# Performance work log

Hardware: AMD Instinct MI355X
Metric: run time of the kernel (lower is better)

Reference implementation:

```python
import jax, jax.numpy as jnp
import numpy as np

VOCAB, D, H1, H2, T = 32000, 256, 256, 256, 12
PAD, START, STOP = 0, 10, 11
B, S, NS = 32, 512, 16


def setup_inputs() -> dict:
    key = jax.random.key(0)
    ks = jax.random.split(key, 16)
    def rn(k, shape, scale=0.1):
        return (jax.random.normal(k, shape) * scale).astype(jnp.float32)
    inputs = jax.random.randint(ks[0], (B, S), 0, VOCAB)
    sent_embs = jax.random.normal(ks[1], (B, NS, 2 * H1), dtype=jnp.float32)
    embed = rn(ks[2], (VOCAB, D)).at[0].set(0.0)  # padding_idx=0
    # BiLSTM 1: input D, hidden H1; gate order i,f,g,o; dim 0 = [fwd, bwd]
    lstm1_wih = rn(ks[3], (2, 4 * H1, D))
    lstm1_whh = rn(ks[4], (2, 4 * H1, H1))
    lstm1_b = rn(ks[5], (2, 4 * H1))  # b_ih + b_hh fused
    # BiLSTM 2: input 4*H1 (= 2*2*lstm1_units), hidden H2
    lstm2_wih = rn(ks[6], (2, 4 * H2, 4 * H1))
    lstm2_whh = rn(ks[7], (2, 4 * H2, H2))
    lstm2_b = rn(ks[8], (2, 4 * H2))
    attW = rn(ks[9], (2 * H1, 2 * H1))
    h2t_w = rn(ks[10], (T, 2 * H2))
    h2t_b = rn(ks[11], (T,))
    trans = jax.random.normal(ks[12], (T, T), dtype=jnp.float32)
    trans = trans.at[START, :].set(-10000.0).at[:, STOP].set(-10000.0)
    return dict(inputs=inputs, sent_embs=sent_embs, embed=embed,
                lstm1_wih=lstm1_wih, lstm1_whh=lstm1_whh, lstm1_b=lstm1_b,
                lstm2_wih=lstm2_wih, lstm2_whh=lstm2_whh, lstm2_b=lstm2_b,
                attW=attW, h2t_w=h2t_w, h2t_b=h2t_b, trans=trans)


def _lstm_dir(x, wih, whh, b, reverse=False):
    # x: (S, B, Din) -> (S, B, H)
    if reverse:
        x = x[::-1]
    Hh = whh.shape[1]
    Bn = x.shape[1]
    def step(carry, xt):
        h, c = carry
        gates = xt @ wih.T + h @ whh.T + b
        i, f, g, o = jnp.split(gates, 4, axis=-1)
        c = jax.nn.sigmoid(f) * c + jax.nn.sigmoid(i) * jnp.tanh(g)
        h = jax.nn.sigmoid(o) * jnp.tanh(c)
        return (h, c), h
    init = (jnp.zeros((Bn, Hh), x.dtype), jnp.zeros((Bn, Hh), x.dtype))
    _, hs = jax.lax.scan(step, init, x)
    return hs[::-1] if reverse else hs


def _bilstm(x, wih, whh, b):
    fwd = _lstm_dir(x, wih[0], whh[0], b[0])
    bwd = _lstm_dir(x, wih[1], whh[1], b[1], reverse=True)
    return jnp.concatenate([fwd, bwd], axis=-1)


def _lstm_features(inputs, sent_embs, embed, lstm1_wih, lstm1_whh, lstm1_b,
                   lstm2_wih, lstm2_whh, lstm2_b, attW, h2t_w, h2t_b):
    emb = embed[inputs].transpose(1, 0, 2)            # (S,B,D); dropout is identity at eval
    l1 = _bilstm(emb, lstm1_wih, lstm1_whh, lstm1_b)  # (S,B,2H1)
    word = l1.transpose(1, 0, 2)                      # (B,S,2H1)
    wx = jnp.einsum('bse,fe->bsf', word, attW)        # Linear W (no bias)
    scores = jnp.einsum('bsf,bnf->bsn', wx, sent_embs)
    aw = jax.nn.softmax(scores, axis=-1)
    g = jnp.einsum('bsn,bnf->bsf', aw, sent_embs)
    comb = jnp.concatenate([wx, g], axis=-1)          # (B,S,4H1)
    l2 = _bilstm(comb.transpose(1, 0, 2), lstm2_wih, lstm2_whh, lstm2_b)  # (S,B,2H2)
    feats = jnp.einsum('sbf,tf->bst', l2, h2t_w) + h2t_b  # (B,S,T)
    return feats


def _viterbi(feats_b, trans):
    # feats_b: (S,T) -> (path (S,), score)
    init = jnp.full((T,), -10000.0, feats_b.dtype).at[START].set(0.0)
    def step(fv, feat):
        sc = fv[None, :] + trans          # [next, prev]
        bp = jnp.argmax(sc, axis=1)
        return jnp.max(sc, axis=1) + feat, bp
    fv, bps = jax.lax.scan(step, init, feats_b)
    term = fv + trans[STOP]
    best = jnp.argmax(term)
    def back(tag, bp):
        return bp[tag], tag
    _, path = jax.lax.scan(back, best, bps, reverse=True)
    return path, term[best]


def reference(inputs, sent_embs, embed, lstm1_wih, lstm1_whh, lstm1_b,
              lstm2_wih, lstm2_whh, lstm2_b, attW, h2t_w, h2t_b, trans):
    feats = _lstm_features(inputs, sent_embs, embed, lstm1_wih, lstm1_whh, lstm1_b,
                           lstm2_wih, lstm2_whh, lstm2_b, attW, h2t_w, h2t_b)
    paths, _ = jax.vmap(_viterbi, in_axes=(0, None))(feats, trans)
    return paths  # (B,S) predicted tag sequence
```

## Files before the change

kernel.cpp:

```cpp
#include <hip/hip_runtime.h>
#include <hip/hip_bf16.h>

#define BB 32
#define SS 512
#define DD 256
#define HH 256
#define GG 1024
#define MM (SS*BB)
#define NSENT 16
#define TT 12
#define TAG_START 10
#define TAG_STOP 11

typedef unsigned long long u64;
typedef unsigned int u32;

__device__ __forceinline__ float sigm(float x) {
  x = fminf(fmaxf(x, -15.f), 15.f);
  return 1.f / (1.f + __expf(-x));
}
__device__ __forceinline__ float tanh_fast(float x) {
  x = fminf(fmaxf(x, -15.f), 15.f);
  float e = __expf(2.f * x);
  return (e - 1.f) / (e + 1.f);
}

__global__ void embed_kernel(const int* __restrict__ toks, const float* __restrict__ emb,
                             float* __restrict__ X1) {
  int m = blockIdx.x;
  int s = m >> 5, b = m & 31;
  int tok = toks[b * SS + s];
  ((float4*)(X1 + (size_t)m * DD))[threadIdx.x] =
      ((const float4*)(emb + (size_t)tok * DD))[threadIdx.x];
}

__launch_bounds__(256)
__global__ void gemm_nt(const float* __restrict__ A, const float* __restrict__ W_,
                        const float* __restrict__ bias_, float* __restrict__ C_,
                        int K, int lda, int ldw, int ldC, size_t wz, size_t cz) {
  __shared__ float As[16 * 132];
  __shared__ float Ws[16 * 132];
  const float* W = W_ + (size_t)blockIdx.z * wz;
  const float* bias = bias_ ? bias_ + (size_t)blockIdx.z * GG : nullptr;
  float* C = C_ + (size_t)blockIdx.z * cz;
  const int tid = threadIdx.x;
  const int n0 = blockIdx.x * 128, m0 = blockIdx.y * 128;
  const int row = tid & 127, half = tid >> 7;
  const int tx = tid & 15, ty = tid >> 4;
  float acc[8][8] = {};
  const float* Arow = A + (size_t)(m0 + row) * lda;
  const float* Wrow = W + (size_t)(n0 + row) * ldw;
  for (int kk = 0; kk < K; kk += 16) {
    const int kb = half * 8;
    float4 a0 = *(const float4*)(Arow + kk + kb);
    float4 a1 = *(const float4*)(Arow + kk + kb + 4);
    float4 w0 = *(const float4*)(Wrow + kk + kb);
    float4 w1 = *(const float4*)(Wrow + kk + kb + 4);
    As[(kb + 0) * 132 + row] = a0.x; As[(kb + 1) * 132 + row] = a0.y;
    As[(kb + 2) * 132 + row] = a0.z; As[(kb + 3) * 132 + row] = a0.w;
    As[(kb + 4) * 132 + row] = a1.x; As[(kb + 5) * 132 + row] = a1.y;
    As[(kb + 6) * 132 + row] = a1.z; As[(kb + 7) * 132 + row] = a1.w;
    Ws[(kb + 0) * 132 + row] = w0.x; Ws[(kb + 1) * 132 + row] = w0.y;
    Ws[(kb + 2) * 132 + row] = w0.z; Ws[(kb + 3) * 132 + row] = w0.w;
    Ws[(kb + 4) * 132 + row] = w1.x; Ws[(kb + 5) * 132 + row] = w1.y;
    Ws[(kb + 6) * 132 + row] = w1.z; Ws[(kb + 7) * 132 + row] = w1.w;
    __syncthreads();
#pragma unroll
    for (int kl = 0; kl < 16; ++kl) {
      const float4 alo = *(const float4*)&As[kl * 132 + ty * 4];
      const float4 ahi = *(const float4*)&As[kl * 132 + 64 + ty * 4];
      const float4 wlo = *(const float4*)&Ws[kl * 132 + tx * 4];
      const float4 whi = *(const float4*)&Ws[kl * 132 + 64 + tx * 4];
      const float am[8] = {alo.x, alo.y, alo.z, alo.w, ahi.x, ahi.y, ahi.z, ahi.w};
      const float wm[8] = {wlo.x, wlo.y, wlo.z, wlo.w, whi.x, whi.y, whi.z, whi.w};
#pragma unroll
      for (int i = 0; i < 8; ++i)
#pragma unroll
        for (int j = 0; j < 8; ++j) acc[i][j] = fmaf(am[i], wm[j], acc[i][j]);
    }
    __syncthreads();
  }
  float4 blo = make_float4(0.f, 0.f, 0.f, 0.f), bhi = blo;
  if (bias) {
    blo = *(const float4*)(bias + n0 + tx * 4);
    bhi = *(const float4*)(bias + n0 + 64 + tx * 4);
  }
#pragma unroll
  for (int i = 0; i < 8; ++i) {
    const int m = m0 + ((i < 4) ? (ty * 4 + i) : (64 + ty * 4 + i - 4));
    float4 lo = make_float4(acc[i][0] + blo.x, acc[i][1] + blo.y,
                            acc[i][2] + blo.z, acc[i][3] + blo.w);
    float4 hi = make_float4(acc[i][4] + bhi.x, acc[i][5] + bhi.y,
                            acc[i][6] + bhi.z, acc[i][7] + bhi.w);
    *(float4*)(C + (size_t)m * ldC + n0 + tx * 4) = lo;
    *(float4*)(C + (size_t)m * ldC + n0 + 64 + tx * 4) = hi;
  }
}

__global__ void prep_whh(const float* __restrict__ whh1, const float* __restrict__ whh2,
                         float* __restrict__ o1, float* __restrict__ o2) {
  int idx0 = blockIdx.x * 256 + threadIdx.x;
  int layer = idx0 >> 19;
  int idx = idx0 & 524287;
  const float* whh = layer ? whh2 : whh1;
  float* out = layer ? o2 : o1;
  int c    = idx & 3;
  int t    = (idx >> 2) & 255;
  int i4   = (idx >> 10) & 31;
  int sl   = (idx >> 15) & 7;
  int d    = idx >> 18;
  int r    = t & 127;
  int half = t >> 7;
  int g = (r >> 5) * 256 + sl * 32 + (r & 31);
  int k = half * 128 + i4 * 4 + c;
  out[idx] = whh[(size_t)(d * GG + g) * HH + k];
}

__launch_bounds__(256, 1)
__global__ void rec_kernel(const float* __restrict__ Xp, const float* __restrict__ whh_p,
                           float* __restrict__ hist, u64* __restrict__ hx,
                           const float* __restrict__ aw, const float* __restrict__ sentW,
                           int useAtt) {
  __shared__ float h_lds[512];
  __shared__ float p_lds[512];
  const int tid = threadIdx.x;
  const int bid = blockIdx.x;
  const int sl = bid >> 5;
  const int db = bid & 31;
  const int d = db & 1;
  const int bg = db >> 1;
  const int r = tid & 127;
  const int half = tid >> 7;
  const float* wp = whh_p + (size_t)(d * 8 + sl) * 32768;
  float w[128];
#pragma unroll
  for (int i4 = 0; i4 < 32; ++i4) {
    const float4 v = *(const float4*)&wp[(size_t)(i4 * 256 + tid) * 4];
    w[i4 * 4 + 0] = v.x; w[i4 * 4 + 1] = v.y;
    w[i4 * 4 + 2] = v.z; w[i4 * 4 + 3] = v.w;
  }
  const float* XpD = Xp + (size_t)d * MM * GG;
  const int gcol = (r >> 5) * 256 + sl * 32 + (r & 31);
  const int jj = tid & 31, cc = tid >> 5;
  const int histMine = ((r >> 4) == sl);
  float creg = 0.f;
  float swA[8], swB[8];
  if (useAtt) {
    const float* swp = sentW + ((size_t)d * 512 + (size_t)(bg * 2) * 16) * 1024 + gcol;
#pragma unroll
    for (int n = 0; n < 8; ++n) {
      swA[n] = swp[(size_t)(half * 8 + n) * 1024];
      swB[n] = swp[(size_t)(16 + half * 8 + n) * 1024];
    }
  }
  u64* grp[2] = { hx + ((size_t)(0 * 2 + d) * 16 + bg) * 512,
                  hx + ((size_t)(1 * 2 + d) * 16 + bg) * 512 };
#pragma unroll 1
  for (int t = 0; t < SS; ++t) {
    const int s = d ? (SS - 1 - t) : t;
    const int m0 = s * BB + bg * 2;
    float x0 = 0.f, x1 = 0.f;
    if (half == 0) {
      x0 = XpD[(size_t)m0 * GG + gcol];
      x1 = XpD[(size_t)(m0 + 1) * GG + gcol];
    }
    if (useAtt) {
      const float* a0 = aw + (size_t)m0 * 16 + half * 8;
#pragma unroll
      for (int n = 0; n < 8; ++n) {
        x0 = fmaf(a0[n], swA[n], x0);
        x1 = fmaf(a0[16 + n], swB[n], x1);
      }
    }
    u64 w0, w1;
    {
      u64* base = grp[t & 1] + tid * 2;
      w0 = __hip_atomic_load(base + 0, __ATOMIC_RELAXED, __HIP_MEMORY_SCOPE_AGENT);
      w1 = __hip_atomic_load(base + 1, __ATOMIC_RELAXED, __HIP_MEMORY_SCOPE_AGENT);
      while (((u32)(w0 >> 32) != (u32)t) | ((u32)(w1 >> 32) != (u32)t)) {
        __builtin_amdgcn_s_sleep(1);
        w0 = __hip_atomic_load(base + 0, __ATOMIC_RELAXED, __HIP_MEMORY_SCOPE_AGENT);
        w1 = __hip_atomic_load(base + 1, __ATOMIC_RELAXED, __HIP_MEMORY_SCOPE_AGENT);
      }
    }
    *(float2*)&h_lds[tid * 2] = make_float2(__uint_as_float((u32)w0),
                                            __uint_as_float((u32)w1));
    if (histMine && t > 0) {
      const int sp = d ? (SS - t) : (t - 1);
      *(float2*)&hist[(size_t)(sp * BB + bg * 2 + half) * 512 + d * 256 + r * 2] =
          make_float2(__uint_as_float((u32)w0), __uint_as_float((u32)w1));
    }
    __syncthreads();
    {
      const int kb = half * 128;
      float p0a = 0.f, p0b = 0.f, p1a = 0.f, p1b = 0.f;
#pragma unroll
      for (int k8 = 0; k8 < 16; ++k8) {
        const float4 h0a = *(const float4*)&h_lds[kb + k8 * 8];
        const float4 h0b = *(const float4*)&h_lds[kb + k8 * 8 + 4];
        const float4 h1a = *(const float4*)&h_lds[256 + kb + k8 * 8];
        const float4 h1b = *(const float4*)&h_lds[256 + kb + k8 * 8 + 4];
        p0a = fmaf(w[k8*8+0], h0a.x, p0a); p0a = fmaf(w[k8*8+1], h0a.y, p0a);
        p0a = fmaf(w[k8*8+2], h0a.z, p0a); p0a = fmaf(w[k8*8+3], h0a.w, p0a);
        p0b = fmaf(w[k8*8+4], h0b.x, p0b); p0b = fmaf(w[k8*8+5], h0b.y, p0b);
        p0b = fmaf(w[k8*8+6], h0b.z, p0b); p0b = fmaf(w[k8*8+7], h0b.w, p0b);
        p1a = fmaf(w[k8*8+0], h1a.x, p1a); p1a = fmaf(w[k8*8+1], h1a.y, p1a);
        p1a = fmaf(w[k8*8+2], h1a.z, p1a); p1a = fmaf(w[k8*8+3], h1a.w, p1a);
        p1b = fmaf(w[k8*8+4], h1b.x, p1b); p1b = fmaf(w[k8*8+5], h1b.y, p1b);
        p1b = fmaf(w[k8*8+6], h1b.z, p1b); p1b = fmaf(w[k8*8+7], h1b.w, p1b);
      }
      *(float2*)&p_lds[tid * 2] = make_float2(p0a + p0b + x0, p1a + p1b + x1);
    }
    __syncthreads();
    if (tid < 64) {
      const float iv = p_lds[(jj) * 2 + cc]       + p_lds[(128 + jj) * 2 + cc];
      const float fv = p_lds[(32 + jj) * 2 + cc]  + p_lds[(128 + 32 + jj) * 2 + cc];
      const float gv = p_lds[(64 + jj) * 2 + cc]  + p_lds[(128 + 64 + jj) * 2 + cc];
      const float ov = p_lds[(96 + jj) * 2 + cc]  + p_lds[(128 + 96 + jj) * 2 + cc];
      const float cs = sigm(fv) * creg + sigm(iv) * tanh_fast(gv);
      creg = cs;
      const float hn = sigm(ov) * tanh_fast(cs);
      u64 wv = ((u64)(u32)(t + 1) << 32) | (u64)__float_as_uint(hn);
      __hip_atomic_store(grp[(t + 1) & 1] + cc * 256 + sl * 32 + jj, wv,
                         __ATOMIC_RELAXED, __HIP_MEMORY_SCOPE_AGENT);
    }
  }
  if (histMine) {
    u64* base = grp[SS & 1] + tid * 2;
    u64 w0, w1;
    do {
      w0 = __hip_atomic_load(base + 0, __ATOMIC_RELAXED, __HIP_MEMORY_SCOPE_AGENT);
      w1 = __hip_atomic_load(base + 1, __ATOMIC_RELAXED, __HIP_MEMORY_SCOPE_AGENT);
      if (((u32)(w0 >> 32) == (u32)SS) & ((u32)(w1 >> 32) == (u32)SS)) break;
      __builtin_amdgcn_s_sleep(1);
    } while (true);
    const int sp = d ? 0 : (SS - 1);
    *(float2*)&hist[(size_t)(sp * BB + bg * 2 + half) * 512 + d * 256 + r * 2] =
        make_float2(__uint_as_float((u32)w0), __uint_as_float((u32)w1));
  }
}

__global__ void aw_kernel(const float* __restrict__ wx, const float* __restrict__ sent,
                          float* __restrict__ awout) {
  __shared__ float sl[NSENT * 512];
  __shared__ float wxr[512];
  __shared__ float parts[256];
  __shared__ float avals[NSENT];
  __shared__ float red0;
  const int tid = threadIdx.x;
  const int b = blockIdx.y;
  const int s0 = blockIdx.x * 32;
  for (int i = tid; i < NSENT * 512; i += 256) sl[i] = sent[(size_t)b * NSENT * 512 + i];
  __syncthreads();
  for (int si = 0; si < 32; ++si) {
    const int m = (s0 + si) * BB + b;
    for (int i = tid; i < 512; i += 256) wxr[i] = wx[(size_t)m * 512 + i];
    __syncthreads();
    const int n = tid >> 4, kp = tid & 15;
    float p = 0.f;
#pragma unroll 8
    for (int f = kp * 32; f < kp * 32 + 32; ++f) p = fmaf(wxr[f], sl[n * 512 + f], p);
    parts[tid] = p;
    __syncthreads();
    if (tid < NSENT) {
      float sc = 0.f;
      for (int qq = 0; qq < 16; ++qq) sc += parts[tid * 16 + qq];
      avals[tid] = sc;
    }
    __syncthreads();
    if (tid == 0) {
      float mx = avals[0];
      for (int qq = 1; qq < NSENT; ++qq) mx = fmaxf(mx, avals[qq]);
      float sm = 0.f;
      for (int qq = 0; qq < NSENT; ++qq) { float e = expf(avals[qq] - mx); avals[qq] = e; sm += e; }
      red0 = 1.f / sm;
    }
    __syncthreads();
    if (tid < NSENT) awout[(size_t)m * 16 + tid] = avals[tid] * red0;
    __syncthreads();
  }
}

__global__ void feats_kernel(const float* __restrict__ l2m, const float* __restrict__ w,
                             const float* __restrict__ bias, float* __restrict__ feats) {
  const int wave = threadIdx.x >> 6, lane = threadIdx.x & 63;
  const int m = blockIdx.x * 4 + wave;
  const float* row = l2m + (size_t)m * 512;
  float rv[8];
#pragma unroll
  for (int i = 0; i < 8; ++i) rv[i] = row[lane + i * 64];
  for (int t = 0; t < TT; ++t) {
    const float* wr = w + t * 512;
    float p = 0.f;
#pragma unroll
    for (int i = 0; i < 8; ++i) p = fmaf(rv[i], wr[lane + i * 64], p);
#pragma unroll
    for (int off = 32; off; off >>= 1) p += __shfl_down(p, off);
    if (lane == 0) feats[(size_t)m * TT + t] = p + bias[t];
  }
}

__global__ void viterbi_kernel(const float* __restrict__ feats, const float* __restrict__ trans,
                               int* __restrict__ out) {
  __shared__ float flds[SS * TT];
  __shared__ unsigned char bp[SS * TT];
  __shared__ float tr[TT * TT];
  __shared__ float fv[TT];
  __shared__ float tv[TT];
  __shared__ int pathS[SS];
  const int b = blockIdx.x, tid = threadIdx.x;
  for (int i = tid; i < SS * TT; i += 64) {
    int s = i / TT, t = i - s * TT;
    flds[i] = feats[(size_t)(s * BB + b) * TT + t];
  }
  for (int i = tid; i < TT * TT; i += 64) tr[i] = trans[i];
  if (tid < TT) fv[tid] = (tid == TAG_START) ? 0.f : -10000.f;
  __syncthreads();
  for (int s = 0; s < SS; ++s) {
    float nf = 0.f;
    if (tid < TT) {
      float mx = -1e30f;
      int bj = 0;
#pragma unroll
      for (int jj = 0; jj < TT; ++jj) {
        float v = fv[jj] + tr[tid * TT + jj];
        if (v > mx) { mx = v; bj = jj; }
      }
      nf = mx + flds[s * TT + tid];
      bp[s * TT + tid] = (unsigned char)bj;
    }
    __syncthreads();
    if (tid < TT) fv[tid] = nf;
    __syncthreads();
  }
  if (tid < TT) tv[tid] = fv[tid] + tr[TAG_STOP * TT + tid];
  __syncthreads();
  if (tid == 0) {
    int best = 0;
    float mx = tv[0];
    for (int jj = 1; jj < TT; ++jj)
      if (tv[jj] > mx) { mx = tv[jj]; best = jj; }
    pathS[SS - 1] = best;
    for (int s = SS - 1; s > 0; --s) { best = bp[s * TT + best]; pathS[s - 1] = best; }
  }
  __syncthreads();
  for (int s = tid; s < SS; s += 64) out[b * SS + s] = pathS[s];
}

#define OFF_XP    ((size_t)0)
#define OFF_WX    ((size_t)134217728)
#define OFF_L2M   ((size_t)167772160)
#define OFF_WORD  ((size_t)201326592)
#define OFF_WT1   ((size_t)234881024)
#define OFF_WT2   ((size_t)236978176)
#define OFF_FEATS ((size_t)239075328)
#define OFF_HX1   ((size_t)239861760)
#define OFF_HX2   ((size_t)240123904)
#define OFF_SENTW ((size_t)240386048)
#define OFF_AW    ((size_t)244580352)

extern "C" void kernel_launch(void* const* d_in, const int* in_sizes, int n_in,
                              void* d_out, int out_size, void* d_ws, size_t ws_size,
                              hipStream_t stream) {
  const int* inputs  = (const int*)d_in[0];
  const float* sent  = (const float*)d_in[1];
  const float* emb   = (const float*)d_in[2];
  const float* l1wih = (const float*)d_in[3];
  const float* l1whh = (const float*)d_in[4];
  const float* l1b   = (const float*)d_in[5];
  const float* l2wih = (const float*)d_in[6];
  const float* l2whh = (const float*)d_in[7];
  const float* l2b   = (const float*)d_in[8];
  const float* attW  = (const float*)d_in[9];
  const float* h2tw  = (const float*)d_in[10];
  const float* h2tb  = (const float*)d_in[11];
  const float* trans = (const float*)d_in[12];
  int* out = (int*)d_out;
  char* ws = (char*)d_ws;

  float* Xp    = (float*)(ws + OFF_XP);
  float* wx    = (float*)(ws + OFF_WX);
  float* l2m   = (float*)(ws + OFF_L2M);
  float* X1    = l2m;
  float* word  = (float*)(ws + OFF_WORD);
  float* wt1   = (float*)(ws + OFF_WT1);
  float* wt2   = (float*)(ws + OFF_WT2);
  float* feats = (float*)(ws + OFF_FEATS);
  u64* hx1     = (u64*)(ws + OFF_HX1);
  u64* hx2     = (u64*)(ws + OFF_HX2);
  float* sentW = (float*)(ws + OFF_SENTW);
  float* awb   = (float*)(ws + OFF_AW);

  (void)hipMemsetAsync(ws + OFF_HX1, 0, 262144 * 2, stream);

  prep_whh<<<4096, 256, 0, stream>>>(l1whh, l2whh, wt1, wt2);
  gemm_nt<<<dim3(8, 4, 2), 256, 0, stream>>>(sent, l2wih + 512, nullptr, sentW,
                                             512, 512, GG, 1024,
                                             (size_t)GG * GG, (size_t)512 * 1024);
  embed_kernel<<<MM, 64, 0, stream>>>(inputs, emb, X1);
  gemm_nt<<<dim3(8, 128, 2), 256, 0, stream>>>(X1, l1wih, l1b, Xp,
                                               DD, DD, DD, GG,
                                               (size_t)GG * DD, (size_t)MM * GG);
  rec_kernel<<<256, 256, 0, stream>>>(Xp, wt1, word, hx1, nullptr, nullptr, 0);
  gemm_nt<<<dim3(4, 128, 1), 256, 0, stream>>>(word, attW, nullptr, wx,
                                               512, 512, 512, 512, 0, 0);
  aw_kernel<<<dim3(16, 32), 256, 0, stream>>>(wx, sent, awb);
  gemm_nt<<<dim3(8, 128, 2), 256, 0, stream>>>(wx, l2wih, l2b, Xp,
                                               512, 512, GG, GG,
                                               (size_t)GG * GG, (size_t)MM * GG);
  rec_kernel<<<256, 256, 0, stream>>>(Xp, wt2, l2m, hx2, awb, sentW, 1);
  feats_kernel<<<MM / 4, 256, 0, stream>>>(l2m, h2tw, h2tb, feats);
  viterbi_kernel<<<BB, 64, 0, stream>>>(feats, trans, out);
}
```

Baseline: 3.931 ms.

## Process four batch rows per recurrent block and hoist attention add out of recurrence

The recurrent LSTM kernel now handles four batch rows per block instead of two, cutting the grid from 256 to 128 blocks so each step's weight-register reuse doubles and fewer blocks take part in the cross-block handshake. The attention-weighted sentence term is moved out of the serial loop into a separate parallel kernel that adds it into Xp beforehand. The loop also prefetches the next step's Xp inputs, has one wave poll the hidden-state exchange with wide vectorized loads, and uses raw barriers. The cost is an extra pass over Xp and double the FMA work per block on the critical path.

```diff
diff --git a/kernel.cpp b/kernel.cpp
--- a/kernel.cpp
+++ b/kernel.cpp
@@ -116,19 +116,42 @@
   out[idx] = whh[(size_t)(d * GG + g) * HH + k];
 }
 
+__global__ void attadd_kernel(const float* __restrict__ aw, const float* __restrict__ sentW,
+                              float* __restrict__ Xp) {
+  __shared__ float a[NSENT];
+  const int idx = blockIdx.x;
+  const int d = idx >> 14;
+  const int m = idx & (MM - 1);
+  const int b = m & 31;
+  const int tid = threadIdx.x;
+  if (tid < NSENT) a[tid] = aw[(size_t)m * 16 + tid];
+  __syncthreads();
+  const int g = tid * 4;
+  float* xp = Xp + ((size_t)d * MM + m) * GG + g;
+  const float* swp = sentW + ((size_t)d * 512 + b * 16) * 1024 + g;
+  float4 acc = *(const float4*)xp;
+#pragma unroll
+  for (int n = 0; n < NSENT; ++n) {
+    const float4 sw = *(const float4*)&swp[(size_t)n * 1024];
+    acc.x = fmaf(a[n], sw.x, acc.x);
+    acc.y = fmaf(a[n], sw.y, acc.y);
+    acc.z = fmaf(a[n], sw.z, acc.z);
+    acc.w = fmaf(a[n], sw.w, acc.w);
+  }
+  *(float4*)xp = acc;
+}
+
 __launch_bounds__(256, 1)
 __global__ void rec_kernel(const float* __restrict__ Xp, const float* __restrict__ whh_p,
-                           float* __restrict__ hist, u64* __restrict__ hx,
-                           const float* __restrict__ aw, const float* __restrict__ sentW,
-                           int useAtt) {
-  __shared__ float h_lds[512];
-  __shared__ float p_lds[512];
+                           float* __restrict__ hist, u64* __restrict__ hx) {
+  __shared__ float h_lds[1024];
+  __shared__ float p_lds[1024];
   const int tid = threadIdx.x;
   const int bid = blockIdx.x;
-  const int sl = bid >> 5;
-  const int db = bid & 31;
+  const int sl = bid >> 4;
+  const int db = bid & 15;
   const int d = db & 1;
-  const int bg = db >> 1;
+  const int bq = db >> 1;
   const int r = tid & 127;
   const int half = tid >> 7;
   const float* wp = whh_p + (size_t)(d * 8 + sl) * 32768;
@@ -141,102 +164,148 @@
   }
   const float* XpD = Xp + (size_t)d * MM * GG;
   const int gcol = (r >> 5) * 256 + sl * 32 + (r & 31);
-  const int jj = tid & 31, cc = tid >> 5;
-  const int histMine = ((r >> 4) == sl);
+  const int etid = tid - 128;
+  const int ecc = (etid >= 0) ? (etid >> 5) : 0;
+  const int ejj = etid & 31;
   float creg = 0.f;
-  float swA[8], swB[8];
-  if (useAtt) {
-    const float* swp = sentW + ((size_t)d * 512 + (size_t)(bg * 2) * 16) * 1024 + gcol;
-#pragma unroll
-    for (int n = 0; n < 8; ++n) {
-      swA[n] = swp[(size_t)(half * 8 + n) * 1024];
-      swB[n] = swp[(size_t)(16 + half * 8 + n) * 1024];
-    }
-  }
-  u64* grp[2] = { hx + ((size_t)(0 * 2 + d) * 16 + bg) * 512,
-                  hx + ((size_t)(1 * 2 + d) * 16 + bg) * 512 };
+  u64* grp[2] = { hx + ((size_t)(0 * 2 + d) * 8 + bq) * 1024,
+                  hx + ((size_t)(1 * 2 + d) * 8 + bq) * 1024 };
+  float xn0 = 0.f, xn1 = 0.f, xn2 = 0.f, xn3 = 0.f;
+  {
+    const int s0 = d ? (SS - 1) : 0;
+    const int m0 = s0 * BB + bq * 4;
+    if (half == 0) {
+      xn0 = XpD[(size_t)(m0 + 0) * GG + gcol];
+      xn1 = XpD[(size_t)(m0 + 1) * GG + gcol];
+      xn2 = XpD[(size_t)(m0 + 2) * GG + gcol];
+      xn3 = XpD[(size_t)(m0 + 3) * GG + gcol];
+    }
+  }
 #pragma unroll 1
   for (int t = 0; t < SS; ++t) {
-    const int s = d ? (SS - 1 - t) : t;
-    const int m0 = s * BB + bg * 2;
-    float x0 = 0.f, x1 = 0.f;
-    if (half == 0) {
-      x0 = XpD[(size_t)m0 * GG + gcol];
-      x1 = XpD[(size_t)(m0 + 1) * GG + gcol];
-    }
-    if (useAtt) {
-      const float* a0 = aw + (size_t)m0 * 16 + half * 8;
-#pragma unroll
-      for (int n = 0; n < 8; ++n) {
-        x0 = fmaf(a0[n], swA[n], x0);
-        x1 = fmaf(a0[16 + n], swB[n], x1);
+    const float xc0 = xn0, xc1 = xn1, xc2 = xn2, xc3 = xn3;
+    const int tn = (t + 1 < SS) ? (t + 1) : (SS - 1);
+    const int sn = d ? (SS - 1 - tn) : tn;
+    const int m0n = sn * BB + bq * 4;
+    if (tid < 64) {
+      u64 pw[16];
+      u64* base = grp[t & 1] + tid * 16;
+      for (;;) {
+#pragma unroll
+        for (int q = 0; q < 16; ++q)
+          pw[q] = __hip_atomic_load(base + q, __ATOMIC_RELAXED, __HIP_MEMORY_SCOPE_AGENT);
+        bool ok = true;
+#pragma unroll
+        for (int q = 0; q < 16; ++q) ok &= ((u32)(pw[q] >> 32) == (u32)t);
+        if (__all(ok)) break;
+        __builtin_amdgcn_s_sleep(1);
       }
-    }
-    u64 w0, w1;
-    {
-      u64* base = grp[t & 1] + tid * 2;
-      w0 = __hip_atomic_load(base + 0, __ATOMIC_RELAXED, __HIP_MEMORY_SCOPE_AGENT);
-      w1 = __hip_atomic_load(base + 1, __ATOMIC_RELAXED, __HIP_MEMORY_SCOPE_AGENT);
-      while (((u32)(w0 >> 32) != (u32)t) | ((u32)(w1 >> 32) != (u32)t)) {
-        __builtin_amdgcn_s_sleep(1);
-        w0 = __hip_atomic_load(base + 0, __ATOMIC_RELAXED, __HIP_MEMORY_SCOPE_AGENT);
-        w1 = __hip_atomic_load(base + 1, __ATOMIC_RELAXED, __HIP_MEMORY_SCOPE_AGENT);
+      float4 hv0 = make_float4(__uint_as_float((u32)pw[0]),  __uint_as_float((u32)pw[1]),
+                               __uint_as_float((u32)pw[2]),  __uint_as_float((u32)pw[3]));
+      float4 hv1 = make_float4(__uint_as_float((u32)pw[4]),  __uint_as_float((u32)pw[5]),
+                               __uint_as_float((u32)pw[6]),  __uint_as_float((u32)pw[7]));
+      float4 hv2 = make_float4(__uint_as_float((u32)pw[8]),  __uint_as_float((u32)pw[9]),
+                               __uint_as_float((u32)pw[10]), __uint_as_float((u32)pw[11]));
+      float4 hv3 = make_float4(__uint_as_float((u32)pw[12]), __uint_as_float((u32)pw[13]),
+                               __uint_as_float((u32)pw[14]), __uint_as_float((u32)pw[15]));
+      *(float4*)&h_lds[tid * 16 + 0]  = hv0;
+      *(float4*)&h_lds[tid * 16 + 4]  = hv1;
+      *(float4*)&h_lds[tid * 16 + 8]  = hv2;
+      *(float4*)&h_lds[tid * 16 + 12] = hv3;
+      if (t > 0) {
+        const int sp = d ? (SS - t) : (t - 1);
+        const int c = tid >> 4, k0 = (tid & 15) * 16;
+        float* hp = &hist[(size_t)(sp * BB + bq * 4 + c) * 512 + d * 256 + k0];
+        *(float4*)&hp[0]  = hv0;
+        *(float4*)&hp[4]  = hv1;
+        *(float4*)&hp[8]  = hv2;
+        *(float4*)&hp[12] = hv3;
       }
-    }
-    *(float2*)&h_lds[tid * 2] = make_float2(__uint_as_float((u32)w0),
-                                            __uint_as_float((u32)w1));
-    if (histMine && t > 0) {
-      const int sp = d ? (SS - t) : (t - 1);
-      *(float2*)&hist[(size_t)(sp * BB + bg * 2 + half) * 512 + d * 256 + r * 2] =
-          make_float2(__uint_as_float((u32)w0), __uint_as_float((u32)w1));
-    }
-    __syncthreads();
+      xn0 = XpD[(size_t)(m0n + 0) * GG + gcol];
+      xn1 = XpD[(size_t)(m0n + 1) * GG + gcol];
+      xn2 = XpD[(size_t)(m0n + 2) * GG + gcol];
+      xn3 = XpD[(size_t)(m0n + 3) * GG + gcol];
+    } else if (half == 0) {
+      xn0 = XpD[(size_t)(m0n + 0) * GG + gcol];
+      xn1 = XpD[(size_t)(m0n + 1) * GG + gcol];
+      xn2 = XpD[(size_t)(m0n + 2) * GG + gcol];
+      xn3 = XpD[(size_t)(m0n + 3) * GG + gcol];
+    }
+    asm volatile("s_waitcnt lgkmcnt(0)" ::: "memory");
+    __builtin_amdgcn_s_barrier();
+    __builtin_amdgcn_sched_barrier(0);
     {
       const int kb = half * 128;
       float p0a = 0.f, p0b = 0.f, p1a = 0.f, p1b = 0.f;
+      float p2a = 0.f, p2b = 0.f, p3a = 0.f, p3b = 0.f;
 #pragma unroll
       for (int k8 = 0; k8 < 16; ++k8) {
-        const float4 h0a = *(const float4*)&h_lds[kb + k8 * 8];
-        const float4 h0b = *(const float4*)&h_lds[kb + k8 * 8 + 4];
-        const float4 h1a = *(const float4*)&h_lds[256 + kb + k8 * 8];
-        const float4 h1b = *(const float4*)&h_lds[256 + kb + k8 * 8 + 4];
-        p0a = fmaf(w[k8*8+0], h0a.x, p0a); p0a = fmaf(w[k8*8+1], h0a.y, p0a);
-        p0a = fmaf(w[k8*8+2], h0a.z, p0a); p0a = fmaf(w[k8*8+3], h0a.w, p0a);
-        p0b = fmaf(w[k8*8+4], h0b.x, p0b); p0b = fmaf(w[k8*8+5], h0b.y, p0b);
-        p0b = fmaf(w[k8*8+6], h0b.z, p0b); p0b = fmaf(w[k8*8+7], h0b.w, p0b);
-        p1a = fmaf(w[k8*8+0], h1a.x, p1a); p1a = fmaf(w[k8*8+1], h1a.y, p1a);
-        p1a = fmaf(w[k8*8+2], h1a.z, p1a); p1a = fmaf(w[k8*8+3], h1a.w, p1a);
-        p1b = fmaf(w[k8*8+4], h1b.x, p1b); p1b = fmaf(w[k8*8+5], h1b.y, p1b);
-        p1b = fmaf(w[k8*8+6], h1b.z, p1b); p1b = fmaf(w[k8*8+7], h1b.w, p1b);
+        const float4 hA0 = *(const float4*)&h_lds[kb + k8 * 8];
+        const float4 hB0 = *(const float4*)&h_lds[kb + k8 * 8 + 4];
+        const float4 hA1 = *(const float4*)&h_lds[256 + kb + k8 * 8];
+        const float4 hB1 = *(const float4*)&h_lds[256 + kb + k8 * 8 + 4];
+        const float4 hA2 = *(const float4*)&h_lds[512 + kb + k8 * 8];
+        const float4 hB2 = *(const float4*)&h_lds[512 + kb + k8 * 8 + 4];
+        const float4 hA3 = *(const float4*)&h_lds[768 + kb + k8 * 8];
+        const float4 hB3 = *(const float4*)&h_lds[768 + kb + k8 * 8 + 4];
+        p0a = fmaf(w[k8*8+0], hA0.x, p0a); p0a = fmaf(w[k8*8+1], hA0.y, p0a);
+        p0a = fmaf(w[k8*8+2], hA0.z, p0a); p0a = fmaf(w[k8*8+3], hA0.w, p0a);
+        p0b = fmaf(w[k8*8+4], hB0.x, p0b); p0b = fmaf(w[k8*8+5], hB0.y, p0b);
+        p0b = fmaf(w[k8*8+6], hB0.z, p0b); p0b = fmaf(w[k8*8+7], hB0.w, p0b);
+        p1a = fmaf(w[k8*8+0], hA1.x, p1a); p1a = fmaf(w[k8*8+1], hA1.y, p1a);
+        p1a = fmaf(w[k8*8+2], hA1.z, p1a); p1a = fmaf(w[k8*8+3], hA1.w, p1a);
+        p1b = fmaf(w[k8*8+4], hB1.x, p1b); p1b = fmaf(w[k8*8+5], hB1.y, p1b);
+        p1b = fmaf(w[k8*8+6], hB1.z, p1b); p1b = fmaf(w[k8*8+7], hB1.w, p1b);
+        p2a = fmaf(w[k8*8+0], hA2.x, p2a); p2a = fmaf(w[k8*8+1], hA2.y, p2a);
+        p2a = fmaf(w[k8*8+2], hA2.z, p2a); p2a = fmaf(w[k8*8+3], hA2.w, p2a);
+        p2b = fmaf(w[k8*8+4], hB2.x, p2b); p2b = fmaf(w[k8*8+5], hB2.y, p2b);
+        p2b = fmaf(w[k8*8+6], hB2.z, p2b); p2b = fmaf(w[k8*8+7], hB2.w, p2b);
+        p3a = fmaf(w[k8*8+0], hA3.x, p3a); p3a = fmaf(w[k8*8+1], hA3.y, p3a);
+        p3a = fmaf(w[k8*8+2], hA3.z, p3a); p3a = fmaf(w[k8*8+3], hA3.w, p3a);
+        p3b = fmaf(w[k8*8+4], hB3.x, p3b); p3b = fmaf(w[k8*8+5], hB3.y, p3b);
+        p3b = fmaf(w[k8*8+6], hB3.z, p3b); p3b = fmaf(w[k8*8+7], hB3.w, p3b);
       }
-      *(float2*)&p_lds[tid * 2] = make_float2(p0a + p0b + x0, p1a + p1b + x1);
-    }
-    __syncthreads();
-    if (tid < 64) {
-      const float iv = p_lds[(jj) * 2 + cc]       + p_lds[(128 + jj) * 2 + cc];
-      const float fv = p_lds[(32 + jj) * 2 + cc]  + p_lds[(128 + 32 + jj) * 2 + cc];
-      const float gv = p_lds[(64 + jj) * 2 + cc]  + p_lds[(128 + 64 + jj) * 2 + cc];
-      const float ov = p_lds[(96 + jj) * 2 + cc]  + p_lds[(128 + 96 + jj) * 2 + cc];
+      *(float4*)&p_lds[tid * 4] = make_float4(p0a + p0b + xc0, p1a + p1b + xc1,
+                                              p2a + p2b + xc2, p3a + p3b + xc3);
+    }
+    asm volatile("s_waitcnt lgkmcnt(0)" ::: "memory");
+    __builtin_amdgcn_s_barrier();
+    __builtin_amdgcn_sched_barrier(0);
+    if (etid >= 0) {
+      const float iv = p_lds[(ejj) * 4 + ecc]      + p_lds[(128 + ejj) * 4 + ecc];
+      const float fv = p_lds[(32 + ejj) * 4 + ecc] + p_lds[(160 + ejj) * 4 + ecc];
+      const float gv = p_lds[(64 + ejj) * 4 + ecc] + p_lds[(192 + ejj) * 4 + ecc];
+      const float ov = p_lds[(96 + ejj) * 4 + ecc] + p_lds[(224 + ejj) * 4 + ecc];
       const float cs = sigm(fv) * creg + sigm(iv) * tanh_fast(gv);
       creg = cs;
       const float hn = sigm(ov) * tanh_fast(cs);
       u64 wv = ((u64)(u32)(t + 1) << 32) | (u64)__float_as_uint(hn);
-      __hip_atomic_store(grp[(t + 1) & 1] + cc * 256 + sl * 32 + jj, wv,
+      __hip_atomic_store(grp[(t + 1) & 1] + ecc * 256 + sl * 32 + ejj, wv,
                          __ATOMIC_RELAXED, __HIP_MEMORY_SCOPE_AGENT);
     }
   }
-  if (histMine) {
-    u64* base = grp[SS & 1] + tid * 2;
-    u64 w0, w1;
-    do {
-      w0 = __hip_atomic_load(base + 0, __ATOMIC_RELAXED, __HIP_MEMORY_SCOPE_AGENT);
-      w1 = __hip_atomic_load(base + 1, __ATOMIC_RELAXED, __HIP_MEMORY_SCOPE_AGENT);
-      if (((u32)(w0 >> 32) == (u32)SS) & ((u32)(w1 >> 32) == (u32)SS)) break;
+  if (tid < 64) {
+    u64 pw[16];
+    u64* base = grp[SS & 1] + tid * 16;
+    for (;;) {
+#pragma unroll
+      for (int q = 0; q < 16; ++q)
+        pw[q] = __hip_atomic_load(base + q, __ATOMIC_RELAXED, __HIP_MEMORY_SCOPE_AGENT);
+      bool ok = true;
+#pragma unroll
+      for (int q = 0; q < 16; ++q) ok &= ((u32)(pw[q] >> 32) == (u32)SS);
+      if (__all(ok)) break;
       __builtin_amdgcn_s_sleep(1);
-    } while (true);
+    }
     const int sp = d ? 0 : (SS - 1);
-    *(float2*)&hist[(size_t)(sp * BB + bg * 2 + half) * 512 + d * 256 + r * 2] =
-        make_float2(__uint_as_float((u32)w0), __uint_as_float((u32)w1));
+    const int c = tid >> 4, k0 = (tid & 15) * 16;
+    float* hp = &hist[(size_t)(sp * BB + bq * 4 + c) * 512 + d * 256 + k0];
+#pragma unroll
+    for (int q = 0; q < 16; q += 4)
+      *(float4*)&hp[q] = make_float4(__uint_as_float((u32)pw[q]),
+                                     __uint_as_float((u32)pw[q + 1]),
+                                     __uint_as_float((u32)pw[q + 2]),
+                                     __uint_as_float((u32)pw[q + 3]));
   }
 }
 
@@ -401,14 +470,15 @@
   gemm_nt<<<dim3(8, 128, 2), 256, 0, stream>>>(X1, l1wih, l1b, Xp,
                                                DD, DD, DD, GG,
                                                (size_t)GG * DD, (size_t)MM * GG);
-  rec_kernel<<<256, 256, 0, stream>>>(Xp, wt1, word, hx1, nullptr, nullptr, 0);
+  rec_kernel<<<128, 256, 0, stream>>>(Xp, wt1, word, hx1);
   gemm_nt<<<dim3(4, 128, 1), 256, 0, stream>>>(word, attW, nullptr, wx,
                                                512, 512, 512, 512, 0, 0);
   aw_kernel<<<dim3(16, 32), 256, 0, stream>>>(wx, sent, awb);
   gemm_nt<<<dim3(8, 128, 2), 256, 0, stream>>>(wx, l2wih, l2b, Xp,
                                                512, 512, GG, GG,
                                                (size_t)GG * GG, (size_t)MM * GG);
-  rec_kernel<<<256, 256, 0, stream>>>(Xp, wt2, l2m, hx2, awb, sentW, 1);
+  attadd_kernel<<<2 * MM, 256, 0, stream>>>(awb, sentW, Xp);
+  rec_kernel<<<128, 256, 0, stream>>>(Xp, wt2, l2m, hx2);
   feats_kernel<<<MM / 4, 256, 0, stream>>>(l2m, h2tw, h2tb, feats);
   viterbi_kernel<<<BB, 64, 0, stream>>>(feats, trans, out);
 }
```

New measurement: 8.438 ms. 2.15x slower.

## Prefetch next-step Xp, defer attention loads, and spin without sleep in LSTM recurrence

Applied to the files above, without the earlier changes.

Loads the precomputed input projection for step t+1 during step t, so global latency is hidden behind the recurrent matvec instead of sitting on the serial critical path. Attention-weight loads are issued after the spin-wait and consumed after the matvec. The spin loop now polls without s_sleep, and __syncthreads is replaced by an explicit lgkmcnt wait plus s_barrier with a scheduling barrier. This trades extra registers and more memory polling traffic for lower per-step latency. The barrier waits only on lgkmcnt, so correctness depends on vector-memory stores to hist not needing ordering at that point.

```diff
diff --git a/kernel.cpp b/kernel.cpp
--- a/kernel.cpp
+++ b/kernel.cpp
@@ -155,32 +155,39 @@
   }
   u64* grp[2] = { hx + ((size_t)(0 * 2 + d) * 16 + bg) * 512,
                   hx + ((size_t)(1 * 2 + d) * 16 + bg) * 512 };
+  float xn0 = 0.f, xn1 = 0.f;
+  if (half == 0) {
+    const int s0 = d ? (SS - 1) : 0;
+    const int m00 = s0 * BB + bg * 2;
+    xn0 = XpD[(size_t)m00 * GG + gcol];
+    xn1 = XpD[(size_t)(m00 + 1) * GG + gcol];
+  }
 #pragma unroll 1
   for (int t = 0; t < SS; ++t) {
-    const int s = d ? (SS - 1 - t) : t;
-    const int m0 = s * BB + bg * 2;
-    float x0 = 0.f, x1 = 0.f;
-    if (half == 0) {
-      x0 = XpD[(size_t)m0 * GG + gcol];
-      x1 = XpD[(size_t)(m0 + 1) * GG + gcol];
-    }
-    if (useAtt) {
-      const float* a0 = aw + (size_t)m0 * 16 + half * 8;
-#pragma unroll
-      for (int n = 0; n < 8; ++n) {
-        x0 = fmaf(a0[n], swA[n], x0);
-        x1 = fmaf(a0[16 + n], swB[n], x1);
-      }
-    }
+    float x0 = xn0, x1 = xn1;
     u64 w0, w1;
     {
       u64* base = grp[t & 1] + tid * 2;
-      w0 = __hip_atomic_load(base + 0, __ATOMIC_RELAXED, __HIP_MEMORY_SCOPE_AGENT);
-      w1 = __hip_atomic_load(base + 1, __ATOMIC_RELAXED, __HIP_MEMORY_SCOPE_AGENT);
-      while (((u32)(w0 >> 32) != (u32)t) | ((u32)(w1 >> 32) != (u32)t)) {
-        __builtin_amdgcn_s_sleep(1);
+      do {
         w0 = __hip_atomic_load(base + 0, __ATOMIC_RELAXED, __HIP_MEMORY_SCOPE_AGENT);
         w1 = __hip_atomic_load(base + 1, __ATOMIC_RELAXED, __HIP_MEMORY_SCOPE_AGENT);
+      } while (((u32)(w0 >> 32) != (u32)t) | ((u32)(w1 >> 32) != (u32)t));
+    }
+    const int s = d ? (SS - 1 - t) : t;
+    const int m0 = s * BB + bg * 2;
+    float av0[8], av1[8];
+    if (useAtt) {
+      const float* a0 = aw + (size_t)m0 * 16 + half * 8;
+#pragma unroll
+      for (int n = 0; n < 8; ++n) { av0[n] = a0[n]; av1[n] = a0[16 + n]; }
+    }
+    {
+      const int tn = (t + 1 < SS) ? (t + 1) : (SS - 1);
+      const int sn = d ? (SS - 1 - tn) : tn;
+      const int m0n = sn * BB + bg * 2;
+      if (half == 0) {
+        xn0 = XpD[(size_t)m0n * GG + gcol];
+        xn1 = XpD[(size_t)(m0n + 1) * GG + gcol];
       }
     }
     *(float2*)&h_lds[tid * 2] = make_float2(__uint_as_float((u32)w0),
@@ -190,7 +197,9 @@
       *(float2*)&hist[(size_t)(sp * BB + bg * 2 + half) * 512 + d * 256 + r * 2] =
           make_float2(__uint_as_float((u32)w0), __uint_as_float((u32)w1));
     }
-    __syncthreads();
+    asm volatile("s_waitcnt lgkmcnt(0)" ::: "memory");
+    __builtin_amdgcn_s_barrier();
+    __builtin_amdgcn_sched_barrier(0);
     {
       const int kb = half * 128;
       float p0a = 0.f, p0b = 0.f, p1a = 0.f, p1b = 0.f;
@@ -209,9 +218,18 @@
         p1b = fmaf(w[k8*8+4], h1b.x, p1b); p1b = fmaf(w[k8*8+5], h1b.y, p1b);
         p1b = fmaf(w[k8*8+6], h1b.z, p1b); p1b = fmaf(w[k8*8+7], h1b.w, p1b);
       }
+      if (useAtt) {
+#pragma unroll
+        for (int n = 0; n < 8; ++n) {
+          x0 = fmaf(av0[n], swA[n], x0);
+          x1 = fmaf(av1[n], swB[n], x1);
+        }
+      }
       *(float2*)&p_lds[tid * 2] = make_float2(p0a + p0b + x0, p1a + p1b + x1);
     }
-    __syncthreads();
+    asm volatile("s_waitcnt lgkmcnt(0)" ::: "memory");
+    __builtin_amdgcn_s_barrier();
+    __builtin_amdgcn_sched_barrier(0);
     if (tid < 64) {
       const float iv = p_lds[(jj) * 2 + cc]       + p_lds[(128 + jj) * 2 + cc];
       const float fv = p_lds[(32 + jj) * 2 + cc]  + p_lds[(128 + 32 + jj) * 2 + cc];
```

Result: slower. 6.978 ms (+77.5%).
